# Performance work log

Hardware: AMD Instinct MI355X
Metric: run time of the kernel (lower is better)

The kernel has to match this reference:

```python
import jax, jax.numpy as jnp
import numpy as np

N, E, D, H, L, G = 50000, 800000, 128, 8, 3, 64
C = D // H  # per-head dim


def setup_inputs() -> dict:
    key = jax.random.key(0)
    ks = jax.random.split(key, 10)
    s = 1.0 / np.sqrt(D)  # glorot-ish scale
    return {
        "x": jax.random.normal(ks[0], (N, D), jnp.float32),
        "edge_index": jax.random.randint(ks[1], (2, E), 0, N, jnp.int32),
        "batch": jnp.sort(jax.random.randint(ks[2], (N,), 0, G, jnp.int32)),
        "Wq": jax.random.normal(ks[3], (L, D, D), jnp.float32) * s,
        "bq": jnp.zeros((L, D), jnp.float32),
        "Wk": jax.random.normal(ks[4], (L, D, D), jnp.float32) * s,
        "bk": jnp.zeros((L, D), jnp.float32),
        "Wv": jax.random.normal(ks[5], (L, D, D), jnp.float32) * s,
        "bv": jnp.zeros((L, D), jnp.float32),
        "Ws": jax.random.normal(ks[6], (L, D, D), jnp.float32) * s,
        "bs": jnp.zeros((L, D), jnp.float32),
        "w_gate": jax.random.normal(ks[7], (D, 1), jnp.float32) * s,
        "b_gate": jnp.zeros((1,), jnp.float32),
    }


def transformer_conv(x, src, dst, Wq, bq, Wk, bk, Wv, bv, Ws, bs):
    # PyG TransformerConv (concat=True, root_weight=True, no edge_attr, eval mode)
    n = x.shape[0]
    q = (x @ Wq + bq).reshape(n, H, C)
    k = (x @ Wk + bk).reshape(n, H, C)
    v = (x @ Wv + bv).reshape(n, H, C)
    # attention logits per edge: [E, H]
    alpha = jnp.einsum('ehc,ehc->eh', q[dst], k[src]) / np.sqrt(C).astype(np.float32)
    # segment softmax over incoming edges of each destination node
    amax = jax.ops.segment_max(alpha, dst, num_segments=n)          # [N, H]
    ea = jnp.exp(alpha - amax[dst])
    denom = jax.ops.segment_sum(ea, dst, num_segments=n)            # [N, H]
    attn = ea / (denom[dst] + 1e-16)                                # [E, H]
    msg = v[src] * attn[:, :, None]                                 # [E, H, C]
    out = jax.ops.segment_sum(msg, dst, num_segments=n).reshape(n, H * C)
    return out + x @ Ws + bs                                        # skip connection


def reference(x, edge_index, batch, Wq, bq, Wk, bk, Wv, bv, Ws, bs, w_gate, b_gate):
    src, dst = edge_index[0], edge_index[1]
    for l in range(L):
        x = transformer_conv(x, src, dst, Wq[l], bq[l], Wk[l], bk[l],
                             Wv[l], bv[l], Ws[l], bs[l])
    # ReadoutPhase: gated sum pool || max pool
    score = jax.nn.sigmoid(x @ w_gate + b_gate)                     # [N, 1]
    pool_sum = jax.ops.segment_sum(score * x, batch, num_segments=G)
    pool_max = jax.ops.segment_max(x, batch, num_segments=G)
    return jnp.concatenate([pool_sum, pool_max], axis=1)            # [G, 2D]
```

## Files before the change

kernel.cpp:

```cpp
#include <hip/hip_runtime.h>
#include <hip/hip_bf16.h>

#define NN 50000
#define EE 800000
#define GG 64
#define PCH 16
#define SCB ((NN + 255) / 256)

typedef __attribute__((ext_vector_type(8)))  short          s16x8;
typedef __attribute__((ext_vector_type(8)))  unsigned short u16x8;
typedef __attribute__((ext_vector_type(16))) float          f32x16;

union BFU { __hip_bfloat16 h; unsigned short u; };
__device__ __forceinline__ unsigned short f2bf(float f) {
    BFU b; b.h = __float2bfloat16(f); return b.u;
}
#define B2F_LO(u) __uint_as_float((u) << 16)
#define B2F_HI(u) __uint_as_float((u) & 0xffff0000u)
#define BF2F(us)  __uint_as_float(((unsigned)(us)) << 16)

__global__ __launch_bounds__(256) void hist_kernel(const int* __restrict__ dst,
                                                   int* __restrict__ counts) {
    int e = blockIdx.x * 256 + threadIdx.x;
    if (e < EE) atomicAdd(&counts[dst[e]], 1);
}

__global__ __launch_bounds__(256)
void node_prep(const int* __restrict__ counts, int* __restrict__ offsets,
               int* __restrict__ gcur,
               const int* __restrict__ batch, int* __restrict__ starts) {
    __shared__ int sm[256];
    __shared__ int base;
    const int t = threadIdx.x;
    const int i = blockIdx.x * 256 + t;
    const int v = (i < NN) ? counts[i] : 0;
    sm[t] = v;
    __syncthreads();
    for (int off = 1; off < 256; off <<= 1) {
        int val = (t >= off) ? sm[t - off] : 0;
        __syncthreads();
        sm[t] += val;
        __syncthreads();
    }
    if (t == 255) base = atomicAdd(gcur, sm[255]);
    __syncthreads();
    if (i < NN) offsets[i] = base + sm[t] - v;
    if (i <= NN) {
        int b  = (i < NN) ? batch[i] : GG;
        int bp = (i == 0) ? -1 : batch[i - 1];
        for (int g = bp + 1; g <= b && g <= GG; ++g) starts[g] = i;
    }
}

__global__ __launch_bounds__(256) void scatter_kernel(const int* __restrict__ src,
                                                      const int* __restrict__ dst,
                                                      const int* __restrict__ offs,
                                                      int* __restrict__ cursor,
                                                      int* __restrict__ csrc) {
    int e = blockIdx.x * 256 + threadIdx.x;
    if (e < EE) {
        int dn = dst[e];
        int p = atomicAdd(&cursor[dn], 1);
        csrc[offs[dn] + p] = src[e];
    }
}

__global__ __launch_bounds__(256)
void prep_weights(const float* __restrict__ Wq, const float* __restrict__ Wk,
                  const float* __restrict__ Wv, const float* __restrict__ Ws,
                  unsigned short* __restrict__ wfh, unsigned short* __restrict__ wfl) {
    const int mat = blockIdx.x;
    const int l = mat >> 2, m = mat & 3;
    const float* W;
    switch (m) {
        case 0:  W = Wq; break;
        case 1:  W = Wk; break;
        case 2:  W = Wv; break;
        default: W = Ws; break;
    }
    W += (size_t)l * 16384;
    const int t = threadIdx.x;
    const int col = blockIdx.y * 16 + (t >> 4);
    const int kk  = t & 15;
    u16x8 hi, lo;
    #pragma unroll
    for (int j = 0; j < 8; ++j) {
        float w = W[(kk * 8 + j) * 128 + col];
        unsigned short uh = f2bf(w);
        hi[j] = uh;
        lo[j] = f2bf(w - BF2F(uh));
    }
    const size_t o = (size_t)mat * 16384 + ((size_t)kk * 128 + col) * 8;
    *(u16x8*)(wfh + o) = hi;
    *(u16x8*)(wfl + o) = lo;
}

__global__ __launch_bounds__(256)
void gemm_mfma(const float* __restrict__ xin,
               const unsigned short* __restrict__ wHg,
               const unsigned short* __restrict__ wLg,
               const float* __restrict__ bq, const float* __restrict__ bk,
               const float* __restrict__ bv, const float* __restrict__ bs,
               unsigned short* __restrict__ qbf, unsigned short* __restrict__ kvb,
               float* __restrict__ xs) {
    __shared__ unsigned short xl[16384];
    const int t = threadIdx.x;
    const int n0 = blockIdx.x * 64;

    const float4* X4 = (const float4*)xin;
    for (int i = t; i < 1024; i += 256) {
        const int row = i >> 4, ch = i & 15;
        const int node = n0 + row;
        float4 fa = make_float4(0.f, 0.f, 0.f, 0.f);
        float4 fb = make_float4(0.f, 0.f, 0.f, 0.f);
        if (node < NN) { fa = X4[node * 32 + ch * 2]; fb = X4[node * 32 + ch * 2 + 1]; }
        const float fv[8] = {fa.x, fa.y, fa.z, fa.w, fb.x, fb.y, fb.z, fb.w};
        u16x8 hi, lo;
        #pragma unroll
        for (int j = 0; j < 8; ++j) {
            unsigned short uh = f2bf(fv[j]);
            hi[j] = uh;
            lo[j] = f2bf(fv[j] - BF2F(uh));
        }
        const int base = row * 128 + (ch ^ (row & 7)) * 8;
        *(u16x8*)&xl[base] = hi;
        *(u16x8*)&xl[8192 + base] = lo;
    }
    __syncthreads();

    const int lane = t & 63, wid = t >> 6;
    const int r = lane & 31, g = lane >> 5;
    const int nt = (wid & 1) * 32;
    const int cb = (wid >> 1) * 64;
    s16x8 ah[8], al[8];
    {
        const int row = nt + r;
        const int s = row & 7;
        const int rb = row * 128;
        #pragma unroll
        for (int kc = 0; kc < 8; ++kc) {
            const int idx = rb + (((kc << 1) | g) ^ s) * 8;
            ah[kc] = *(const s16x8*)&xl[idx];
            al[kc] = *(const s16x8*)&xl[8192 + idx];
        }
    }
    const int col0 = cb + r, col1 = cb + 32 + r;

    #pragma unroll
    for (int pm = 0; pm < 2; ++pm) {
        const int m = pm ? 3 : 0;
        const unsigned short* WH = wHg + m * 16384;
        const unsigned short* WL = wLg + m * 16384;
        f32x16 acc0, acc1;
        #pragma unroll
        for (int j = 0; j < 16; ++j) { acc0[j] = 0.f; acc1[j] = 0.f; }
        #pragma unroll
        for (int kc = 0; kc < 8; ++kc) {
            const int kk = (kc << 1) | g;
            const s16x8 b0 = *(const s16x8*)&WH[(kk * 128 + col0) * 8];
            const s16x8 b1 = *(const s16x8*)&WH[(kk * 128 + col1) * 8];
            const s16x8 c0 = *(const s16x8*)&WL[(kk * 128 + col0) * 8];
            const s16x8 c1 = *(const s16x8*)&WL[(kk * 128 + col1) * 8];
            acc0 = __builtin_amdgcn_mfma_f32_32x32x16_bf16(ah[kc], b0, acc0, 0, 0, 0);
            acc1 = __builtin_amdgcn_mfma_f32_32x32x16_bf16(ah[kc], b1, acc1, 0, 0, 0);
            acc0 = __builtin_amdgcn_mfma_f32_32x32x16_bf16(al[kc], b0, acc0, 0, 0, 0);
            acc1 = __builtin_amdgcn_mfma_f32_32x32x16_bf16(al[kc], b1, acc1, 0, 0, 0);
            acc0 = __builtin_amdgcn_mfma_f32_32x32x16_bf16(ah[kc], c0, acc0, 0, 0, 0);
            acc1 = __builtin_amdgcn_mfma_f32_32x32x16_bf16(ah[kc], c1, acc1, 0, 0, 0);
        }
        const float* bp = pm ? bs : bq;
        const float b0 = bp[col0], b1 = bp[col1];
        if (pm == 0) {
            #pragma unroll
            for (int reg = 0; reg < 16; ++reg) {
                const int node = n0 + nt + (reg & 3) + 8 * (reg >> 2) + 4 * g;
                if (node < NN) {
                    unsigned short* qrow = qbf + (size_t)node * 128;
                    qrow[col0] = f2bf(acc0[reg] + b0);
                    qrow[col1] = f2bf(acc1[reg] + b1);
                }
            }
        } else {
            #pragma unroll
            for (int reg = 0; reg < 16; ++reg) {
                const int node = n0 + nt + (reg & 3) + 8 * (reg >> 2) + 4 * g;
                if (node < NN) {
                    xs[node * 128 + col0] = acc0[reg] + b0;
                    xs[node * 128 + col1] = acc1[reg] + b1;
                }
            }
        }
    }

    {
        const unsigned short* WK = wHg + 1 * 16384;
        const unsigned short* WV = wHg + 2 * 16384;
        f32x16 ak0, ak1, av0, av1;
        #pragma unroll
        for (int j = 0; j < 16; ++j) { ak0[j] = 0.f; ak1[j] = 0.f; av0[j] = 0.f; av1[j] = 0.f; }
        #pragma unroll
        for (int kc = 0; kc < 8; ++kc) {
            const int kk = (kc << 1) | g;
            const s16x8 k0 = *(const s16x8*)&WK[(kk * 128 + col0) * 8];
            const s16x8 k1 = *(const s16x8*)&WK[(kk * 128 + col1) * 8];
            const s16x8 v0 = *(const s16x8*)&WV[(kk * 128 + col0) * 8];
            const s16x8 v1 = *(const s16x8*)&WV[(kk * 128 + col1) * 8];
            ak0 = __builtin_amdgcn_mfma_f32_32x32x16_bf16(ah[kc], k0, ak0, 0, 0, 0);
            ak1 = __builtin_amdgcn_mfma_f32_32x32x16_bf16(ah[kc], k1, ak1, 0, 0, 0);
            av0 = __builtin_amdgcn_mfma_f32_32x32x16_bf16(ah[kc], v0, av0, 0, 0, 0);
            av1 = __builtin_amdgcn_mfma_f32_32x32x16_bf16(ah[kc], v1, av1, 0, 0, 0);
        }
        const float bk0 = bk[col0], bk1 = bk[col1];
        const float bv0 = bv[col0], bv1 = bv[col1];
        const int k0o = (col0 >> 4) * 32 + (col0 & 15);
        const int k1o = (col1 >> 4) * 32 + (col1 & 15);
        #pragma unroll
        for (int reg = 0; reg < 16; ++reg) {
            const int node = n0 + nt + (reg & 3) + 8 * (reg >> 2) + 4 * g;
            if (node < NN) {
                unsigned short* row = kvb + (size_t)node * 256;
                row[k0o]      = f2bf(ak0[reg] + bk0);
                row[k1o]      = f2bf(ak1[reg] + bk1);
                row[k0o + 16] = f2bf(av0[reg] + bv0);
                row[k1o + 16] = f2bf(av1[reg] + bv1);
            }
        }
    }
}

__global__ __launch_bounds__(256)
void attn_kernel(const unsigned short* __restrict__ qbf, const uint4* __restrict__ kv4,
                 float* __restrict__ xio,
                 const int* __restrict__ offs, const int* __restrict__ cnts,
                 const int* __restrict__ csrc) {
    const int t = threadIdx.x;
    const int h = t & 7;
    const int quarter = (t >> 3) & 3;
    const int n = blockIdx.x * 8 + (t >> 5);
    const uint4* qp = (const uint4*)(qbf + (size_t)n * 128) + h * 2;
    const uint4 qA = qp[0], qB = qp[1];
    const float4 q0 = make_float4(B2F_LO(qA.x), B2F_HI(qA.x), B2F_LO(qA.y), B2F_HI(qA.y));
    const float4 q1 = make_float4(B2F_LO(qA.z), B2F_HI(qA.z), B2F_LO(qA.w), B2F_HI(qA.w));
    const float4 q2 = make_float4(B2F_LO(qB.x), B2F_HI(qB.x), B2F_LO(qB.y), B2F_HI(qB.y));
    const float4 q3 = make_float4(B2F_LO(qB.z), B2F_HI(qB.z), B2F_LO(qB.w), B2F_HI(qB.w));
    float m = -__builtin_inff();
    float d = 0.f;
    float4 a0 = {}, a1 = {}, a2 = {}, a3 = {};
    const int e0 = offs[n], e1 = e0 + cnts[n];
    const int estart = e0 + quarter;
    if (estart < e1) {
        uint4 ka, kb, va, vb;
        { const uint4* p = kv4 + (size_t)csrc[estart] * 32 + h * 4;
          ka = p[0]; kb = p[1]; va = p[2]; vb = p[3]; }
        uint4 na, nb, nc, nd;
        if (estart + 4 < e1) {
            const uint4* p = kv4 + (size_t)csrc[estart + 4] * 32 + h * 4;
            na = p[0]; nb = p[1]; nc = p[2]; nd = p[3];
        }
        for (int ec = estart; ec < e1; ec += 4) {
            uint4 fa, fb, fc, fd;
            if (ec + 8 < e1) {
                const uint4* p = kv4 + (size_t)csrc[ec + 8] * 32 + h * 4;
                fa = p[0]; fb = p[1]; fc = p[2]; fd = p[3];
            }
            float dot =
                q0.x * B2F_LO(ka.x) + q0.y * B2F_HI(ka.x) + q0.z * B2F_LO(ka.y) + q0.w * B2F_HI(ka.y)
              + q1.x * B2F_LO(ka.z) + q1.y * B2F_HI(ka.z) + q1.z * B2F_LO(ka.w) + q1.w * B2F_HI(ka.w)
              + q2.x * B2F_LO(kb.x) + q2.y * B2F_HI(kb.x) + q2.z * B2F_LO(kb.y) + q2.w * B2F_HI(kb.y)
              + q3.x * B2F_LO(kb.z) + q3.y * B2F_HI(kb.z) + q3.z * B2F_LO(kb.w) + q3.w * B2F_HI(kb.w);
            const float alpha = dot * 0.25f;
            const float nm = fmaxf(m, alpha);
            const float scale = __expf(m - nm);
            const float p = __expf(alpha - nm);
            d = d * scale + p;
            a0.x = a0.x * scale + p * B2F_LO(va.x); a0.y = a0.y * scale + p * B2F_HI(va.x);
            a0.z = a0.z * scale + p * B2F_LO(va.y); a0.w = a0.w * scale + p * B2F_HI(va.y);
            a1.x = a1.x * scale + p * B2F_LO(va.z); a1.y = a1.y * scale + p * B2F_HI(va.z);
            a1.z = a1.z * scale + p * B2F_LO(va.w); a1.w = a1.w * scale + p * B2F_HI(va.w);
            a2.x = a2.x * scale + p * B2F_LO(vb.x); a2.y = a2.y * scale + p * B2F_HI(vb.x);
            a2.z = a2.z * scale + p * B2F_LO(vb.y); a2.w = a2.w * scale + p * B2F_HI(vb.y);
            a3.x = a3.x * scale + p * B2F_LO(vb.z); a3.y = a3.y * scale + p * B2F_HI(vb.z);
            a3.z = a3.z * scale + p * B2F_LO(vb.w); a3.w = a3.w * scale + p * B2F_HI(vb.w);
            m = nm;
            ka = na; kb = nb; va = nc; vb = nd;
            na = fa; nb = fb; nc = fc; nd = fd;
        }
    }
    #pragma unroll
    for (int o = 8; o <= 16; o <<= 1) {
        const float mp = __shfl_xor(m, o);
        const float dp = __shfl_xor(d, o);
        const float mc = fmaxf(fmaxf(m, mp), -1e30f);
        const float s0 = __expf(m - mc);
        const float s1 = __expf(mp - mc);
        d = d * s0 + dp * s1;
        float pa;
        pa = __shfl_xor(a0.x, o); a0.x = a0.x * s0 + pa * s1;
        pa = __shfl_xor(a0.y, o); a0.y = a0.y * s0 + pa * s1;
        pa = __shfl_xor(a0.z, o); a0.z = a0.z * s0 + pa * s1;
        pa = __shfl_xor(a0.w, o); a0.w = a0.w * s0 + pa * s1;
        pa = __shfl_xor(a1.x, o); a1.x = a1.x * s0 + pa * s1;
        pa = __shfl_xor(a1.y, o); a1.y = a1.y * s0 + pa * s1;
        pa = __shfl_xor(a1.z, o); a1.z = a1.z * s0 + pa * s1;
        pa = __shfl_xor(a1.w, o); a1.w = a1.w * s0 + pa * s1;
        pa = __shfl_xor(a2.x, o); a2.x = a2.x * s0 + pa * s1;
        pa = __shfl_xor(a2.y, o); a2.y = a2.y * s0 + pa * s1;
        pa = __shfl_xor(a2.z, o); a2.z = a2.z * s0 + pa * s1;
        pa = __shfl_xor(a2.w, o); a2.w = a2.w * s0 + pa * s1;
        pa = __shfl_xor(a3.x, o); a3.x = a3.x * s0 + pa * s1;
        pa = __shfl_xor(a3.y, o); a3.y = a3.y * s0 + pa * s1;
        pa = __shfl_xor(a3.z, o); a3.z = a3.z * s0 + pa * s1;
        pa = __shfl_xor(a3.w, o); a3.w = a3.w * s0 + pa * s1;
        m = mc;
    }
    if (quarter == 0) {
        const float inv = 1.f / (d + 1e-16f);
        float4* op = (float4*)(xio + (size_t)n * 128 + h * 16);
        float4 o0 = op[0], o1 = op[1], o2 = op[2], o3 = op[3];
        o0.x += a0.x * inv; o0.y += a0.y * inv; o0.z += a0.z * inv; o0.w += a0.w * inv;
        o1.x += a1.x * inv; o1.y += a1.y * inv; o1.z += a1.z * inv; o1.w += a1.w * inv;
        o2.x += a2.x * inv; o2.y += a2.y * inv; o2.z += a2.z * inv; o2.w += a2.w * inv;
        o3.x += a3.x * inv; o3.y += a3.y * inv; o3.z += a3.z * inv; o3.w += a3.w * inv;
        op[0] = o0; op[1] = o1; op[2] = o2; op[3] = o3;
    }
}

__global__ __launch_bounds__(128)
void pool_partial(const float* __restrict__ x, const float* __restrict__ wg,
                  const float* __restrict__ bg, const int* __restrict__ starts,
                  float* __restrict__ psum, float* __restrict__ pmax) {
    const int g  = blockIdx.x / PCH;
    const int ch = blockIdx.x % PCH;
    const int c  = threadIdx.x;
    const int s0 = starts[g], s1 = starts[g + 1];
    const int total = s1 - s0;
    const int len = (total + PCH - 1) / PCH;
    const int n0 = s0 + ch * len;
    const int n1 = min(n0 + len, s1);
    const float w = wg[c];
    const float b = bg[0];
    __shared__ float red[2];
    float sum = 0.f, mx = -__builtin_inff();
    for (int n = n0; n < n1; ++n) {
        const float xv = x[n * 128 + c];
        float p = xv * w;
        #pragma unroll
        for (int o = 32; o; o >>= 1) p += __shfl_xor(p, o);
        if ((c & 63) == 0) red[c >> 6] = p;
        __syncthreads();
        const float dot = red[0] + red[1];
        __syncthreads();
        const float score = 1.f / (1.f + __expf(-(dot + b)));
        sum += score * xv;
        mx = fmaxf(mx, xv);
    }
    psum[blockIdx.x * 128 + c] = sum;
    pmax[blockIdx.x * 128 + c] = mx;
}

__global__ __launch_bounds__(128)
void pool_final(const float* __restrict__ psum, const float* __restrict__ pmax,
                float* __restrict__ out) {
    const int g = blockIdx.x, c = threadIdx.x;
    float s = 0.f, m = -__builtin_inff();
    #pragma unroll
    for (int ch = 0; ch < PCH; ++ch) {
        s += psum[(g * PCH + ch) * 128 + c];
        m = fmaxf(m, pmax[(g * PCH + ch) * 128 + c]);
    }
    out[g * 256 + c] = s;
    out[g * 256 + 128 + c] = m;
}

extern "C" void kernel_launch(void* const* d_in, const int* in_sizes, int n_in,
                              void* d_out, int out_size, void* d_ws, size_t ws_size,
                              hipStream_t stream) {
    const float* x     = (const float*)d_in[0];
    const int*   ei    = (const int*)d_in[1];
    const int*   batch = (const int*)d_in[2];
    const float* Wq = (const float*)d_in[3];
    const float* bq = (const float*)d_in[4];
    const float* Wk = (const float*)d_in[5];
    const float* bk = (const float*)d_in[6];
    const float* Wv = (const float*)d_in[7];
    const float* bv = (const float*)d_in[8];
    const float* Ws = (const float*)d_in[9];
    const float* bs = (const float*)d_in[10];
    const float* wg = (const float*)d_in[11];
    const float* bg = (const float*)d_in[12];
    float* out = (float*)d_out;

    char* w = (char*)d_ws;
    unsigned short* qbf  = (unsigned short*)w; w += (size_t)NN * 128 * 2;
    unsigned short* kvb  = (unsigned short*)w; w += (size_t)NN * 256 * 2;
    float* bufA          = (float*)w;          w += (size_t)NN * 128 * 4;
    float* bufB          = (float*)w;          w += (size_t)NN * 128 * 4;
    float* psum          = (float*)w;          w += (size_t)GG * PCH * 128 * 4;
    float* pmax          = (float*)w;          w += (size_t)GG * PCH * 128 * 4;
    unsigned short* wfh  = (unsigned short*)w; w += (size_t)12 * 16384 * 2;
    unsigned short* wfl  = (unsigned short*)w; w += (size_t)12 * 16384 * 2;
    int* counts          = (int*)w;            w += (size_t)NN * 4;
    int* cursor          = (int*)w;            w += (size_t)NN * 4;
    int* gcur            = (int*)w;            w += (size_t)64 * 4;
    const size_t zero_bytes = (size_t)(NN + NN + 64) * 4;
    int* offsets         = (int*)w;            w += (size_t)NN * 4;
    int* csrc            = (int*)w;            w += (size_t)EE * 4;
    int* starts          = (int*)w;            w += (size_t)(GG + 1) * 4;

    const int* srcI = ei;
    const int* dstI = ei + EE;

    hipMemsetAsync(counts, 0, zero_bytes, stream);
    hist_kernel<<<(EE + 255) / 256, 256, 0, stream>>>(dstI, counts);
    node_prep<<<SCB, 256, 0, stream>>>(counts, offsets, gcur, batch, starts);
    scatter_kernel<<<(EE + 255) / 256, 256, 0, stream>>>(srcI, dstI, offsets, cursor, csrc);
    prep_weights<<<dim3(12, 8), 256, 0, stream>>>(Wq, Wk, Wv, Ws, wfh, wfl);

    const float* xin = x;
    float* bufs[2] = {bufA, bufB};
    const int gemmBlocks = (NN + 63) / 64;
    const int attnBlocks = NN / 8;
    for (int l = 0; l < 3; ++l) {
        float* xs = bufs[l & 1];
        gemm_mfma<<<gemmBlocks, 256, 0, stream>>>(
            xin, wfh + (size_t)l * 4 * 16384, wfl + (size_t)l * 4 * 16384,
            bq + (size_t)l * 128, bk + (size_t)l * 128,
            bv + (size_t)l * 128, bs + (size_t)l * 128,
            qbf, kvb, xs);
        attn_kernel<<<attnBlocks, 256, 0, stream>>>(qbf, (const uint4*)kvb, xs, offsets, counts, csrc);
        xin = xs;
    }

    pool_partial<<<GG * PCH, 128, 0, stream>>>(xin, wg, bg, starts, psum, pmax);
    pool_final<<<GG, 128, 0, stream>>>(psum, pmax, out);
}
```

Baseline: 431.5 us.

## Shrink GEMM tile to 32 nodes and prefetch weight fragments per k-step

The projection GEMM now handles 32 nodes per block instead of 64, with each wave covering one 32-column tile instead of two, which halves LDS use and register pressure and doubles the number of blocks. A-fragments are read from LDS inside the k-loop rather than preloaded into registers, and the B-fragments for the next k-step are software-prefetched from global memory. The aim is higher occupancy and better latency hiding. In exchange, each weight fragment is fetched from global/L2 by twice as many blocks, and LDS reads move into the inner loop.

```diff
diff --git a/kernel.cpp b/kernel.cpp
--- a/kernel.cpp
+++ b/kernel.cpp
@@ -103,12 +103,12 @@
                const float* __restrict__ bv, const float* __restrict__ bs,
                unsigned short* __restrict__ qbf, unsigned short* __restrict__ kvb,
                float* __restrict__ xs) {
-    __shared__ unsigned short xl[16384];
+    __shared__ unsigned short xl[8192];
     const int t = threadIdx.x;
-    const int n0 = blockIdx.x * 64;
+    const int n0 = blockIdx.x * 32;
 
     const float4* X4 = (const float4*)xin;
-    for (int i = t; i < 1024; i += 256) {
+    for (int i = t; i < 512; i += 256) {
         const int row = i >> 4, ch = i & 15;
         const int node = n0 + row;
         float4 fa = make_float4(0.f, 0.f, 0.f, 0.f);
@@ -124,70 +124,53 @@
         }
         const int base = row * 128 + (ch ^ (row & 7)) * 8;
         *(u16x8*)&xl[base] = hi;
-        *(u16x8*)&xl[8192 + base] = lo;
+        *(u16x8*)&xl[4096 + base] = lo;
     }
     __syncthreads();
 
     const int lane = t & 63, wid = t >> 6;
     const int r = lane & 31, g = lane >> 5;
-    const int nt = (wid & 1) * 32;
-    const int cb = (wid >> 1) * 64;
-    s16x8 ah[8], al[8];
-    {
-        const int row = nt + r;
-        const int s = row & 7;
-        const int rb = row * 128;
-        #pragma unroll
-        for (int kc = 0; kc < 8; ++kc) {
-            const int idx = rb + (((kc << 1) | g) ^ s) * 8;
-            ah[kc] = *(const s16x8*)&xl[idx];
-            al[kc] = *(const s16x8*)&xl[8192 + idx];
-        }
-    }
-    const int col0 = cb + r, col1 = cb + 32 + r;
+    const int col0 = wid * 32 + r;
+    const int arb = r * 128, ars = r & 7;
 
     #pragma unroll
     for (int pm = 0; pm < 2; ++pm) {
         const int m = pm ? 3 : 0;
         const unsigned short* WH = wHg + m * 16384;
         const unsigned short* WL = wLg + m * 16384;
-        f32x16 acc0, acc1;
-        #pragma unroll
-        for (int j = 0; j < 16; ++j) { acc0[j] = 0.f; acc1[j] = 0.f; }
+        f32x16 acc;
+        #pragma unroll
+        for (int j = 0; j < 16; ++j) acc[j] = 0.f;
+        s16x8 b = *(const s16x8*)&WH[((((0 << 1) | g) * 128) + col0) * 8];
+        s16x8 c = *(const s16x8*)&WL[((((0 << 1) | g) * 128) + col0) * 8];
         #pragma unroll
         for (int kc = 0; kc < 8; ++kc) {
-            const int kk = (kc << 1) | g;
-            const s16x8 b0 = *(const s16x8*)&WH[(kk * 128 + col0) * 8];
-            const s16x8 b1 = *(const s16x8*)&WH[(kk * 128 + col1) * 8];
-            const s16x8 c0 = *(const s16x8*)&WL[(kk * 128 + col0) * 8];
-            const s16x8 c1 = *(const s16x8*)&WL[(kk * 128 + col1) * 8];
-            acc0 = __builtin_amdgcn_mfma_f32_32x32x16_bf16(ah[kc], b0, acc0, 0, 0, 0);
-            acc1 = __builtin_amdgcn_mfma_f32_32x32x16_bf16(ah[kc], b1, acc1, 0, 0, 0);
-            acc0 = __builtin_amdgcn_mfma_f32_32x32x16_bf16(al[kc], b0, acc0, 0, 0, 0);
-            acc1 = __builtin_amdgcn_mfma_f32_32x32x16_bf16(al[kc], b1, acc1, 0, 0, 0);
-            acc0 = __builtin_amdgcn_mfma_f32_32x32x16_bf16(ah[kc], c0, acc0, 0, 0, 0);
-            acc1 = __builtin_amdgcn_mfma_f32_32x32x16_bf16(ah[kc], c1, acc1, 0, 0, 0);
-        }
-        const float* bp = pm ? bs : bq;
-        const float b0 = bp[col0], b1 = bp[col1];
+            s16x8 nb, nc;
+            if (kc < 7) {
+                const int nkk = ((kc + 1) << 1) | g;
+                nb = *(const s16x8*)&WH[(nkk * 128 + col0) * 8];
+                nc = *(const s16x8*)&WL[(nkk * 128 + col0) * 8];
+            }
+            const int idx = arb + ((((kc << 1) | g) ^ ars) * 8);
+            const s16x8 a_h = *(const s16x8*)&xl[idx];
+            const s16x8 a_l = *(const s16x8*)&xl[4096 + idx];
+            acc = __builtin_amdgcn_mfma_f32_32x32x16_bf16(a_h, b, acc, 0, 0, 0);
+            acc = __builtin_amdgcn_mfma_f32_32x32x16_bf16(a_l, b, acc, 0, 0, 0);
+            acc = __builtin_amdgcn_mfma_f32_32x32x16_bf16(a_h, c, acc, 0, 0, 0);
+            b = nb; c = nc;
+        }
+        const float bb = (pm ? bs : bq)[col0];
         if (pm == 0) {
             #pragma unroll
             for (int reg = 0; reg < 16; ++reg) {
-                const int node = n0 + nt + (reg & 3) + 8 * (reg >> 2) + 4 * g;
-                if (node < NN) {
-                    unsigned short* qrow = qbf + (size_t)node * 128;
-                    qrow[col0] = f2bf(acc0[reg] + b0);
-                    qrow[col1] = f2bf(acc1[reg] + b1);
-                }
+                const int node = n0 + (reg & 3) + 8 * (reg >> 2) + 4 * g;
+                if (node < NN) qbf[(size_t)node * 128 + col0] = f2bf(acc[reg] + bb);
             }
         } else {
             #pragma unroll
             for (int reg = 0; reg < 16; ++reg) {
-                const int node = n0 + nt + (reg & 3) + 8 * (reg >> 2) + 4 * g;
-                if (node < NN) {
-                    xs[node * 128 + col0] = acc0[reg] + b0;
-                    xs[node * 128 + col1] = acc1[reg] + b1;
-                }
+                const int node = n0 + (reg & 3) + 8 * (reg >> 2) + 4 * g;
+                if (node < NN) xs[(size_t)node * 128 + col0] = acc[reg] + bb;
             }
         }
     }
@@ -195,34 +178,34 @@
     {
         const unsigned short* WK = wHg + 1 * 16384;
         const unsigned short* WV = wHg + 2 * 16384;
-        f32x16 ak0, ak1, av0, av1;
-        #pragma unroll
-        for (int j = 0; j < 16; ++j) { ak0[j] = 0.f; ak1[j] = 0.f; av0[j] = 0.f; av1[j] = 0.f; }
+        f32x16 ak, av;
+        #pragma unroll
+        for (int j = 0; j < 16; ++j) { ak[j] = 0.f; av[j] = 0.f; }
+        s16x8 kb0 = *(const s16x8*)&WK[((((0 << 1) | g) * 128) + col0) * 8];
+        s16x8 vb0 = *(const s16x8*)&WV[((((0 << 1) | g) * 128) + col0) * 8];
         #pragma unroll
         for (int kc = 0; kc < 8; ++kc) {
-            const int kk = (kc << 1) | g;
-            const s16x8 k0 = *(const s16x8*)&WK[(kk * 128 + col0) * 8];
-            const s16x8 k1 = *(const s16x8*)&WK[(kk * 128 + col1) * 8];
-            const s16x8 v0 = *(const s16x8*)&WV[(kk * 128 + col0) * 8];
-            const s16x8 v1 = *(const s16x8*)&WV[(kk * 128 + col1) * 8];
-            ak0 = __builtin_amdgcn_mfma_f32_32x32x16_bf16(ah[kc], k0, ak0, 0, 0, 0);
-            ak1 = __builtin_amdgcn_mfma_f32_32x32x16_bf16(ah[kc], k1, ak1, 0, 0, 0);
-            av0 = __builtin_amdgcn_mfma_f32_32x32x16_bf16(ah[kc], v0, av0, 0, 0, 0);
-            av1 = __builtin_amdgcn_mfma_f32_32x32x16_bf16(ah[kc], v1, av1, 0, 0, 0);
-        }
-        const float bk0 = bk[col0], bk1 = bk[col1];
-        const float bv0 = bv[col0], bv1 = bv[col1];
+            s16x8 nk, nv;
+            if (kc < 7) {
+                const int nkk = ((kc + 1) << 1) | g;
+                nk = *(const s16x8*)&WK[(nkk * 128 + col0) * 8];
+                nv = *(const s16x8*)&WV[(nkk * 128 + col0) * 8];
+            }
+            const int idx = arb + ((((kc << 1) | g) ^ ars) * 8);
+            const s16x8 a_h = *(const s16x8*)&xl[idx];
+            ak = __builtin_amdgcn_mfma_f32_32x32x16_bf16(a_h, kb0, ak, 0, 0, 0);
+            av = __builtin_amdgcn_mfma_f32_32x32x16_bf16(a_h, vb0, av, 0, 0, 0);
+            kb0 = nk; vb0 = nv;
+        }
+        const float bk0 = bk[col0], bv0 = bv[col0];
         const int k0o = (col0 >> 4) * 32 + (col0 & 15);
-        const int k1o = (col1 >> 4) * 32 + (col1 & 15);
         #pragma unroll
         for (int reg = 0; reg < 16; ++reg) {
-            const int node = n0 + nt + (reg & 3) + 8 * (reg >> 2) + 4 * g;
+            const int node = n0 + (reg & 3) + 8 * (reg >> 2) + 4 * g;
             if (node < NN) {
                 unsigned short* row = kvb + (size_t)node * 256;
-                row[k0o]      = f2bf(ak0[reg] + bk0);
-                row[k1o]      = f2bf(ak1[reg] + bk1);
-                row[k0o + 16] = f2bf(av0[reg] + bv0);
-                row[k1o + 16] = f2bf(av1[reg] + bv1);
+                row[k0o]      = f2bf(ak[reg] + bk0);
+                row[k0o + 16] = f2bf(av[reg] + bv0);
             }
         }
     }
@@ -418,7 +401,7 @@
 
     const float* xin = x;
     float* bufs[2] = {bufA, bufB};
-    const int gemmBlocks = (NN + 63) / 64;
+    const int gemmBlocks = (NN + 31) / 32;
     const int attnBlocks = NN / 8;
     for (int l = 0; l < 3; ++l) {
         float* xs = bufs[l & 1];
```

Result: no change. 439.0 us (+1.7%).
